# Kernel optimization log

Measured on AMD Instinct MI355X. Metric: run time of the kernel, lower is better.

Reference implementation:

```python
import jax, jax.numpy as jnp
import numpy as np
import math

B, S, D = 4, 4096, 1024
NUM_HEADS = 8  # hardcoded in the original via `// 8` and view(..., 8, head_dim)
HEAD_DIM = D // NUM_HEADS


def setup_inputs() -> dict:
    key = jax.random.key(0)
    ks = jax.random.split(key, 11)
    s = 1.0 / math.sqrt(D)
    inp = {
        "input_seq": jax.random.normal(ks[0], (B, S, D), dtype=jnp.float32),
        # Linear weights stored as [in, out] (y = x @ W + b), matching nn.Linear math
        "Wq": jax.random.uniform(ks[1], (D, D), jnp.float32, -s, s),
        "bq": jax.random.uniform(ks[2], (D,), jnp.float32, -s, s),
        "Wk": jax.random.uniform(ks[3], (D, D), jnp.float32, -s, s),
        "bk": jax.random.uniform(ks[4], (D,), jnp.float32, -s, s),
        "Wv": jax.random.uniform(ks[5], (D, D), jnp.float32, -s, s),
        "bv": jax.random.uniform(ks[6], (D,), jnp.float32, -s, s),
        "W1": jax.random.uniform(ks[7], (D, D), jnp.float32, -s, s),
        "b1": jax.random.uniform(ks[8], (D,), jnp.float32, -s, s),
        "W2": jax.random.uniform(ks[9], (D, D), jnp.float32, -s, s),
        "b2": jax.random.uniform(ks[10], (D,), jnp.float32, -s, s),
    }
    return inp


def reference(input_seq, Wq, bq, Wk, bk, Wv, bv, W1, b1, W2, b2):
    # QKV projections (query=key=input_seq in self-attention)
    q = input_seq @ Wq + bq  # [B,S,D]
    k = input_seq @ Wk + bk
    v = input_seq @ Wv + bv

    # Faithful to the original: view(B, S, 8, head_dim) with NO transpose,
    # so attention is computed over the 8 heads within each token position.
    q = q.reshape(B, S, NUM_HEADS, HEAD_DIM)
    k = k.reshape(B, S, NUM_HEADS, HEAD_DIM)
    v = v.reshape(B, S, NUM_HEADS, HEAD_DIM)

    # scores[b,s,h,t] = q[b,s,h,:] . k[b,s,t,:] / sqrt(head_dim)  -> [B,S,8,8]
    scores = jnp.einsum("bshd,bstd->bsht", q, k) / jnp.sqrt(jnp.float32(HEAD_DIM))
    # dropout on scores before softmax: identity at inference
    attn_weights = jax.nn.softmax(scores, axis=-1)  # [B,S,8,8]

    out = jnp.einsum("bsht,bstd->bshd", attn_weights, v).reshape(B, S, D)
    # dropout on attn_output: identity at inference

    # FFN: Linear -> ReLU -> Linear (no residual / layernorm in the original)
    ff = jnp.maximum(out @ W1 + b1, 0.0) @ W2 + b2
    return ff, attn_weights
```

## Files before the change

### kernel.cpp

```cpp
#include <hip/hip_runtime.h>
#include <hip/hip_bf16.h>


#define DI __device__ __forceinline__

typedef __bf16 bf16raw;
typedef bf16raw bf16x8 __attribute__((ext_vector_type(8)));
typedef float floatx4 __attribute__((ext_vector_type(4)));

DI unsigned short f2bf(float f) {
    __hip_bfloat16 h = __float2bfloat16(f);
    return *reinterpret_cast<unsigned short*>(&h);
}

DI void async16(unsigned short* lds, const unsigned short* g) {
    __builtin_amdgcn_global_load_lds(
        (const __attribute__((address_space(1))) void*)g,
        (__attribute__((address_space(3))) void*)lds,
        16, 0, 0);
}

template <typename T> DI T cvt_out(float v);
template <> DI float cvt_out<float>(float v) { return v; }
template <> DI unsigned short cvt_out<unsigned short>(float v) { return f2bf(v); }

template <int I0, int J0>
DI void mfma16(floatx4 (&acc)[8][4], const bf16x8 (&af)[4][2],
               const bf16x8 (&bf)[2][2]) {
#pragma unroll
    for (int s = 0; s < 2; s++)
#pragma unroll
        for (int i = 0; i < 4; i++)
#pragma unroll
            for (int j = 0; j < 2; j++)
                acc[I0 + i][J0 + j] = __builtin_amdgcn_mfma_f32_16x16x32_bf16(
                    af[i][s], bf[j][s], acc[I0 + i][J0 + j], 0, 0, 0);
}

#define STG_A(b, rb, kt) do { \
    async16(&As[b][(rb) * 64 + wofs], aS + (size_t)(rb) * K + (kt)); \
    async16(&As[b][((rb) + 64) * 64 + wofs], aS + (size_t)((rb) + 64) * K + (kt)); \
} while (0)
#define STG_B(b, rb, kt) do { \
    async16(&Bs[b][(rb) * 64 + wofs], bS + (size_t)(rb) * K + (kt)); \
    async16(&Bs[b][((rb) + 64) * 64 + wofs], bS + (size_t)((rb) + 64) * K + (kt)); \
} while (0)
#define LDA4(dst, b, base) do { _Pragma("unroll") \
    for (int i_ = 0; i_ < 4; i_++) { \
        dst[i_][0] = *reinterpret_cast<const bf16x8*>(&As[b][(base) + i_ * 1024 + sl0]); \
        dst[i_][1] = *reinterpret_cast<const bf16x8*>(&As[b][(base) + i_ * 1024 + sl1]); \
    } } while (0)
#define LDB4(dst, b, base) do { _Pragma("unroll") \
    for (int j_ = 0; j_ < 2; j_++) { \
        dst[j_][0] = *reinterpret_cast<const bf16x8*>(&Bs[b][(base) + j_ * 1024 + sl0]); \
        dst[j_][1] = *reinterpret_cast<const bf16x8*>(&Bs[b][(base) + j_ * 1024 + sl1]); \
    } } while (0)
#define BARRIER __builtin_amdgcn_s_barrier()
#define WAIT_LGKM0 do { asm volatile("s_waitcnt lgkmcnt(0)" ::: "memory"); \
    __builtin_amdgcn_sched_barrier(0); } while (0)
#define VMCNT6 asm volatile("s_waitcnt vmcnt(6)" ::: "memory")

template <int K, int N, int GX, typename OutT, bool RELU>
__global__ __launch_bounds__(512, 2)
void gemm256_bt(const unsigned short* __restrict__ A,
                const unsigned short* __restrict__ Bt,
                const float* __restrict__ bias,
                OutT* __restrict__ C)
{
    constexpr int BK = 64;
    constexpr int NT = K / BK;
    constexpr int NP = NT / 2;
    static_assert(NT % 2 == 0 && N % 256 == 0, "");

    __shared__ unsigned short As[2][256 * BK];
    __shared__ unsigned short Bs[2][256 * BK];

    const int tid  = threadIdx.x;
    const int wave = tid >> 6;
    const int lane = tid & 63;
    const int quad = lane >> 4;
    const int l16  = lane & 15;
    const int sw7  = l16 & 7;
    const int wm   = wave >> 2;
    const int wn   = wave & 3;

    const int g   = blockIdx.x + GX * blockIdx.y;
    const int xcd = g & 7;
    const int t   = g >> 3;
    const int bx  = t % GX;
    const int by  = t / GX + (gridDim.y >> 3) * xcd;
    const int m0  = by * 256;
    const int n0  = bx * 256;

    const int srow = tid >> 3;
    const int soct = ((tid & 7) ^ (srow & 7)) * 8;
    const unsigned short* aS = A  + (size_t)(m0 + srow) * K + soct;
    const unsigned short* bS = Bt + (size_t)(n0 + srow) * K + soct;
    const int wofs = wave * 512;

    const int aro = (wm * 64 + l16) * 64;
    const int bro = (wn * 32 + l16) * 64;
    const int sl0 = (quad ^ sw7) * 8;
    const int sl1 = ((quad + 4) ^ sw7) * 8;

    floatx4 acc[8][4];
    const floatx4 zero = {0.f, 0.f, 0.f, 0.f};
#pragma unroll
    for (int i = 0; i < 8; i++)
#pragma unroll
        for (int j = 0; j < 4; j++) acc[i][j] = zero;

    bf16x8 a0[4][2], a1[4][2], b0[2][2], b1[2][2];

    STG_A(0, 0, 0); STG_B(0, 0, 0); STG_B(0, 128, 0); STG_A(0, 128, 0);
    STG_A(1, 0, BK); STG_B(1, 0, BK); STG_B(1, 128, BK);
    VMCNT6;
    BARRIER;

    for (int it = 0; it < NP; ++it) {
        const int ktA = (2 * it + 1) * BK;
        const int kt2 = ((2 * it + 2) < NT ? (2 * it + 2) : (NT - 1)) * BK;
        const int kt3 = ((2 * it + 3) < NT ? (2 * it + 3) : (NT - 1)) * BK;

        LDA4(a0, 0, aro);
        LDB4(b0, 0, bro);
        STG_A(1, 128, ktA);
        BARRIER; WAIT_LGKM0;
        __builtin_amdgcn_s_setprio(1);
        mfma16<0, 0>(acc, a0, b0);
        __builtin_amdgcn_s_setprio(0);
        BARRIER;

        LDB4(b1, 0, bro + 8192);
        STG_A(0, 0, kt2);
        BARRIER; WAIT_LGKM0;
        __builtin_amdgcn_s_setprio(1);
        mfma16<0, 2>(acc, a0, b1);
        __builtin_amdgcn_s_setprio(0);
        BARRIER;

        LDA4(a1, 0, aro + 8192);
        STG_B(0, 0, kt2);
        BARRIER; WAIT_LGKM0;
        __builtin_amdgcn_s_setprio(1);
        mfma16<4, 0>(acc, a1, b0);
        __builtin_amdgcn_s_setprio(0);
        BARRIER;

        STG_B(0, 128, kt2);
        VMCNT6;
        BARRIER;
        __builtin_amdgcn_s_setprio(1);
        mfma16<4, 2>(acc, a1, b1);
        __builtin_amdgcn_s_setprio(0);
        BARRIER;

        LDA4(a0, 1, aro);
        LDB4(b0, 1, bro);
        STG_A(0, 128, kt2);
        BARRIER; WAIT_LGKM0;
        __builtin_amdgcn_s_setprio(1);
        mfma16<0, 0>(acc, a0, b0);
        __builtin_amdgcn_s_setprio(0);
        BARRIER;

        LDB4(b1, 1, bro + 8192);
        STG_A(1, 0, kt3);
        BARRIER; WAIT_LGKM0;
        __builtin_amdgcn_s_setprio(1);
        mfma16<0, 2>(acc, a0, b1);
        __builtin_amdgcn_s_setprio(0);
        BARRIER;

        LDA4(a1, 1, aro + 8192);
        STG_B(1, 0, kt3);
        BARRIER; WAIT_LGKM0;
        __builtin_amdgcn_s_setprio(1);
        mfma16<4, 0>(acc, a1, b0);
        __builtin_amdgcn_s_setprio(0);
        BARRIER;

        STG_B(1, 128, kt3);
        VMCNT6;
        BARRIER;
        __builtin_amdgcn_s_setprio(1);
        mfma16<4, 2>(acc, a1, b1);
        __builtin_amdgcn_s_setprio(0);
        BARRIER;
    }
    asm volatile("s_waitcnt vmcnt(0)" ::: "memory");

#pragma unroll
    for (int j = 0; j < 4; j++) {
        const int col = n0 + wn * 32 + (j & 1) * 16 + (j >> 1) * 128 + l16;
        const float bv = bias[col];
#pragma unroll
        for (int i = 0; i < 8; i++) {
            const int rb = m0 + wm * 64 + (i & 3) * 16 + (i >> 2) * 128 + quad * 4;
#pragma unroll
            for (int r = 0; r < 4; r++) {
                float v = acc[i][j][r] + bv;
                if (RELU) v = fmaxf(v, 0.f);
                C[(size_t)(rb + r) * N + col] = cvt_out<OutT>(v);
            }
        }
    }
}

#undef STG_A
#undef STG_B
#undef LDA4
#undef LDB4
#undef BARRIER
#undef WAIT_LGKM0
#undef VMCNT6

__global__ void cast_f32_to_bf16(const float* __restrict__ src,
                                 unsigned short* __restrict__ dst, int n4) {
    int i = blockIdx.x * blockDim.x + threadIdx.x;
    if (i < n4) {
        float4 v = reinterpret_cast<const float4*>(src)[i];
        ushort4 o = { f2bf(v.x), f2bf(v.y), f2bf(v.z), f2bf(v.w) };
        reinterpret_cast<ushort4*>(dst)[i] = o;
    }
}

struct WPack {
    const float* src[5];
    unsigned short* dst[5];
};
__global__ void transpose_cast_all(WPack p) {
    __shared__ float tile[32][33];
    const float* W = p.src[blockIdx.z];
    unsigned short* Wt = p.dst[blockIdx.z];
    const int n0 = blockIdx.x * 32, k0 = blockIdx.y * 32;
    const int tx = threadIdx.x, ty = threadIdx.y;
#pragma unroll
    for (int i = 0; i < 32; i += 8)
        tile[ty + i][tx] = W[(size_t)(k0 + ty + i) * 1024 + n0 + tx];
    __syncthreads();
#pragma unroll
    for (int i = 0; i < 32; i += 8)
        Wt[(size_t)(n0 + ty + i) * 1024 + k0 + tx] = f2bf(tile[tx][ty + i]);
}

__global__ void concat_bias(const float* __restrict__ bq,
                            const float* __restrict__ bk,
                            const float* __restrict__ bv,
                            float* __restrict__ dst) {
    int i = blockIdx.x * blockDim.x + threadIdx.x;
    const float* s = (i < 1024) ? bq : ((i < 2048) ? bk : bv);
    dst[i] = s[i & 1023];
}

DI float dot8(unsigned a, unsigned b, float acc) {
    union { unsigned u; float f; } al, ah, bl, bh;
    al.u = a << 16; ah.u = a & 0xffff0000u;
    bl.u = b << 16; bh.u = b & 0xffff0000u;
    return acc + al.f * bl.f + ah.f * bh.f;
}

__global__ __launch_bounds__(256)
void attention_kernel(const unsigned short* __restrict__ qkv,
                      unsigned short* __restrict__ out_bf,
                      float* __restrict__ attn_w)
{
    __shared__ unsigned short sqkv[4][3072];
    __shared__ float sw[4][64];
    const int tid  = threadIdx.x;
    const int wave = tid >> 6;
    const int lane = tid & 63;
    const int m    = blockIdx.x * 4 + wave;

    {
        const uint4* src = reinterpret_cast<const uint4*>(qkv + (size_t)m * 3072);
        uint4* dst = reinterpret_cast<uint4*>(&sqkv[wave][0]);
#pragma unroll
        for (int i = 0; i < 6; i++) dst[lane + 64 * i] = src[lane + 64 * i];
    }
    __syncthreads();

    {
        const int h = lane >> 3, t = lane & 7;
        const uint2* q8 = reinterpret_cast<const uint2*>(&sqkv[wave][h * 128]);
        const uint2* k8 = reinterpret_cast<const uint2*>(&sqkv[wave][1024 + t * 128]);
        float dot = 0.f;
#pragma unroll
        for (int d = 0; d < 32; d++) {
            uint2 a = q8[d], b = k8[d];
            dot = dot8(a.x, b.x, dot);
            dot = dot8(a.y, b.y, dot);
        }
        float score = dot * 0.08838834764831843f;
        float mx = score;
#pragma unroll
        for (int o = 1; o < 8; o <<= 1) mx = fmaxf(mx, __shfl_xor(mx, o, 8));
        float e = __expf(score - mx);
        float sum = e;
#pragma unroll
        for (int o = 1; o < 8; o <<= 1) sum += __shfl_xor(sum, o, 8);
        float w = e / sum;
        sw[wave][lane] = w;
        attn_w[(size_t)m * 64 + lane] = w;
    }
    __syncthreads();

    {
        const int h  = lane >> 3;
        const int d0 = (lane & 7) * 16;
        float acc[16];
#pragma unroll
        for (int i = 0; i < 16; i++) acc[i] = 0.f;
#pragma unroll
        for (int t = 0; t < 8; t++) {
            const float w = sw[wave][h * 8 + t];
            const uint4* v8 = reinterpret_cast<const uint4*>(
                &sqkv[wave][2048 + t * 128 + d0]);
            uint4 v0 = v8[0], v1 = v8[1];
            unsigned vv[8] = { v0.x, v0.y, v0.z, v0.w, v1.x, v1.y, v1.z, v1.w };
#pragma unroll
            for (int i = 0; i < 8; i++) {
                union { unsigned u; float f; } lo, hi;
                lo.u = vv[i] << 16; hi.u = vv[i] & 0xffff0000u;
                acc[i * 2]     += w * lo.f;
                acc[i * 2 + 1] += w * hi.f;
            }
        }
        unsigned o[8];
#pragma unroll
        for (int i = 0; i < 8; i++)
            o[i] = (unsigned)f2bf(acc[i * 2]) | ((unsigned)f2bf(acc[i * 2 + 1]) << 16);
        uint4* dst = reinterpret_cast<uint4*>(out_bf + (size_t)m * 1024 + lane * 16);
        dst[0] = make_uint4(o[0], o[1], o[2], o[3]);
        dst[1] = make_uint4(o[4], o[5], o[6], o[7]);
    }
}

extern "C" void kernel_launch(void* const* d_in, const int* in_sizes, int n_in,
                              void* d_out, int out_size, void* d_ws, size_t ws_size,
                              hipStream_t stream) {
    const float* x  = (const float*)d_in[0];
    const float* Wq = (const float*)d_in[1];
    const float* bq = (const float*)d_in[2];
    const float* Wk = (const float*)d_in[3];
    const float* bk = (const float*)d_in[4];
    const float* Wv = (const float*)d_in[5];
    const float* bv = (const float*)d_in[6];
    const float* W1 = (const float*)d_in[7];
    const float* b1 = (const float*)d_in[8];
    const float* W2 = (const float*)d_in[9];
    const float* b2 = (const float*)d_in[10];

    constexpr int D = 1024;
    constexpr int M = 4 * 4096;
    constexpr size_t XN = (size_t)M * D;

    float* ff_out   = (float*)d_out;
    float* attn_out = (float*)d_out + XN;

    char* ws = (char*)d_ws;
    size_t off = 0;
    auto alloc = [&](size_t bytes) -> char* {
        char* p = ws + off;
        off += (bytes + 255) & ~(size_t)255;
        return p;
    };
    unsigned short* Xbf   = (unsigned short*)alloc(XN * 2);
    unsigned short* Wtqkv = (unsigned short*)alloc((size_t)3 * D * D * 2);
    unsigned short* Wt1   = (unsigned short*)alloc((size_t)D * D * 2);
    unsigned short* Wt2   = (unsigned short*)alloc((size_t)D * D * 2);
    float*          bqkv  = (float*)alloc(3 * D * 4);
    unsigned short* outbf = (unsigned short*)alloc(XN * 2);
    unsigned short* hbf   = (unsigned short*)alloc(XN * 2);
    unsigned short* qkv   = (unsigned short*)alloc((size_t)M * 3 * D * 2);

    cast_f32_to_bf16<<<(int)(XN / 4 / 256), 256, 0, stream>>>(x, Xbf, (int)(XN / 4));
    WPack p;
    p.src[0] = Wq; p.dst[0] = Wtqkv;
    p.src[1] = Wk; p.dst[1] = Wtqkv + (size_t)D * D;
    p.src[2] = Wv; p.dst[2] = Wtqkv + (size_t)2 * D * D;
    p.src[3] = W1; p.dst[3] = Wt1;
    p.src[4] = W2; p.dst[4] = Wt2;
    transpose_cast_all<<<dim3(32, 32, 5), dim3(32, 8), 0, stream>>>(p);
    concat_bias<<<12, 256, 0, stream>>>(bq, bk, bv, bqkv);

    gemm256_bt<D, 3 * D, 12, unsigned short, false>
        <<<dim3(12, 64), 512, 0, stream>>>(Xbf, Wtqkv, bqkv, qkv);
    attention_kernel<<<M / 4, 256, 0, stream>>>(qkv, outbf, attn_out);

    gemm256_bt<D, D, 4, unsigned short, true>
        <<<dim3(4, 64), 512, 0, stream>>>(outbf, Wt1, b1, hbf);
    gemm256_bt<D, D, 4, float, false>
        <<<dim3(4, 64), 512, 0, stream>>>(hbf, Wt2, b2, ff_out);
}
```

Measured before the change: 371.2 us.

## Software-pipeline LDS fragment loads one stage ahead of MFMA in GEMM loop

Restructures the 256x256 bf16 GEMM main loop so the LDS reads for the next MFMA quarter are issued before the current quarter's MFMAs run. Partial lgkmcnt waits (4 or 8 outstanding) replace the full waits, and one barrier per stage replaces two. The aim is to hide LDS read latency and cut barrier stalls between quarters. The prologue now stages a full second buffer and preloads the first fragments. Tighter vmcnt gating and reordered async stores add risk around buffer reuse and correctness at the loop tail.

```diff
diff --git a/kernel.cpp b/kernel.cpp
--- a/kernel.cpp
+++ b/kernel.cpp
@@ -56,9 +56,11 @@
         dst[j_][1] = *reinterpret_cast<const bf16x8*>(&Bs[b][(base) + j_ * 1024 + sl1]); \
     } } while (0)
 #define BARRIER __builtin_amdgcn_s_barrier()
-#define WAIT_LGKM0 do { asm volatile("s_waitcnt lgkmcnt(0)" ::: "memory"); \
+#define LGKM(n) do { asm volatile("s_waitcnt lgkmcnt(" #n ")" ::: "memory"); \
     __builtin_amdgcn_sched_barrier(0); } while (0)
-#define VMCNT6 asm volatile("s_waitcnt vmcnt(6)" ::: "memory")
+#define GATE4 asm volatile("s_waitcnt vmcnt(4)" ::: "memory")
+#define PRIO1 __builtin_amdgcn_s_setprio(1)
+#define PRIO0 __builtin_amdgcn_s_setprio(0)
 
 template <int K, int N, int GX, typename OutT, bool RELU>
 __global__ __launch_bounds__(512, 2)
@@ -110,83 +112,71 @@
 #pragma unroll
         for (int j = 0; j < 4; j++) acc[i][j] = zero;
 
-    bf16x8 a0[4][2], a1[4][2], b0[2][2], b1[2][2];
+    bf16x8 aL[4][2], aH[4][2], bL[2][2], bH[2][2];
 
     STG_A(0, 0, 0); STG_B(0, 0, 0); STG_B(0, 128, 0); STG_A(0, 128, 0);
-    STG_A(1, 0, BK); STG_B(1, 0, BK); STG_B(1, 128, BK);
-    VMCNT6;
+    STG_A(1, 0, BK); STG_B(1, 0, BK); STG_B(1, 128, BK); STG_A(1, 128, BK);
+    asm volatile("s_waitcnt vmcnt(8)" ::: "memory");
     BARRIER;
-
+    LDA4(aL, 0, aro);
+    LDB4(bL, 0, bro);
+    asm volatile("s_waitcnt lgkmcnt(0)" ::: "memory");
+    __builtin_amdgcn_sched_barrier(0);
+
+#pragma unroll 1
     for (int it = 0; it < NP; ++it) {
-        const int ktA = (2 * it + 1) * BK;
         const int kt2 = ((2 * it + 2) < NT ? (2 * it + 2) : (NT - 1)) * BK;
         const int kt3 = ((2 * it + 3) < NT ? (2 * it + 3) : (NT - 1)) * BK;
 
-        LDA4(a0, 0, aro);
-        LDB4(b0, 0, bro);
-        STG_A(1, 128, ktA);
-        BARRIER; WAIT_LGKM0;
-        __builtin_amdgcn_s_setprio(1);
-        mfma16<0, 0>(acc, a0, b0);
-        __builtin_amdgcn_s_setprio(0);
-        BARRIER;
-
-        LDB4(b1, 0, bro + 8192);
+        BARRIER;
+        LDB4(bH, 0, bro + 8192);
         STG_A(0, 0, kt2);
-        BARRIER; WAIT_LGKM0;
-        __builtin_amdgcn_s_setprio(1);
-        mfma16<0, 2>(acc, a0, b1);
-        __builtin_amdgcn_s_setprio(0);
-        BARRIER;
-
-        LDA4(a1, 0, aro + 8192);
+        LGKM(4);
+        PRIO1; mfma16<0, 0>(acc, aL, bL); PRIO0;
+
+        BARRIER;
+        LDA4(aH, 0, aro + 8192);
         STG_B(0, 0, kt2);
-        BARRIER; WAIT_LGKM0;
-        __builtin_amdgcn_s_setprio(1);
-        mfma16<4, 0>(acc, a1, b0);
-        __builtin_amdgcn_s_setprio(0);
-        BARRIER;
-
+        LGKM(8);
+        PRIO1; mfma16<0, 2>(acc, aL, bH); PRIO0;
+
+        GATE4;
+        BARRIER;
+        LDA4(aL, 1, aro);
         STG_B(0, 128, kt2);
-        VMCNT6;
-        BARRIER;
-        __builtin_amdgcn_s_setprio(1);
-        mfma16<4, 2>(acc, a1, b1);
-        __builtin_amdgcn_s_setprio(0);
-        BARRIER;
-
-        LDA4(a0, 1, aro);
-        LDB4(b0, 1, bro);
+        LGKM(8);
+        PRIO1; mfma16<4, 0>(acc, aH, bL); PRIO0;
+
+        BARRIER;
+        LDB4(bL, 1, bro);
         STG_A(0, 128, kt2);
-        BARRIER; WAIT_LGKM0;
-        __builtin_amdgcn_s_setprio(1);
-        mfma16<0, 0>(acc, a0, b0);
-        __builtin_amdgcn_s_setprio(0);
-        BARRIER;
-
-        LDB4(b1, 1, bro + 8192);
+        LGKM(4);
+        PRIO1; mfma16<4, 2>(acc, aH, bH); PRIO0;
+
+        BARRIER;
+        LDB4(bH, 1, bro + 8192);
         STG_A(1, 0, kt3);
-        BARRIER; WAIT_LGKM0;
-        __builtin_amdgcn_s_setprio(1);
-        mfma16<0, 2>(acc, a0, b1);
-        __builtin_amdgcn_s_setprio(0);
-        BARRIER;
-
-        LDA4(a1, 1, aro + 8192);
+        LGKM(4);
+        PRIO1; mfma16<0, 0>(acc, aL, bL); PRIO0;
+
+        BARRIER;
+        LDA4(aH, 1, aro + 8192);
         STG_B(1, 0, kt3);
-        BARRIER; WAIT_LGKM0;
-        __builtin_amdgcn_s_setprio(1);
-        mfma16<4, 0>(acc, a1, b0);
-        __builtin_amdgcn_s_setprio(0);
-        BARRIER;
-
+        LGKM(8);
+        PRIO1; mfma16<0, 2>(acc, aL, bH); PRIO0;
+
+        GATE4;
+        BARRIER;
+        LDA4(aL, 0, aro);
         STG_B(1, 128, kt3);
-        VMCNT6;
-        BARRIER;
-        __builtin_amdgcn_s_setprio(1);
-        mfma16<4, 2>(acc, a1, b1);
-        __builtin_amdgcn_s_setprio(0);
-        BARRIER;
+        LGKM(8);
+        PRIO1; mfma16<4, 0>(acc, aH, bL); PRIO0;
+
+        BARRIER;
+        LDB4(bL, 0, bro);
+        STG_A(1, 128, kt3);
+        LGKM(4);
+        PRIO1; mfma16<4, 2>(acc, aH, bH); PRIO0;
     }
     asm volatile("s_waitcnt vmcnt(0)" ::: "memory");
 
@@ -212,8 +202,10 @@
 #undef LDA4
 #undef LDB4
 #undef BARRIER
-#undef WAIT_LGKM0
-#undef VMCNT6
+#undef LGKM
+#undef GATE4
+#undef PRIO1
+#undef PRIO0
 
 __global__ void cast_f32_to_bf16(const float* __restrict__ src,
                                  unsigned short* __restrict__ dst, int n4) {
```

Result: no change. 371.8 us (+0.2%).
